# Optimization experiments

Measured on AMD Instinct MI355X. Metric: run time of the kernel, lower is better.

The kernel has to match this reference:

```python
import jax, jax.numpy as jnp
import numpy as np

D, H, DH, DF = 128, 8, 16, 512
N_Q, N_KV, E = 20000, 20000, 640000


def _xavier(key, shape):
    fan_in, fan_out = shape[1], shape[0]
    lim = float(np.sqrt(6.0 / (fan_in + fan_out)))
    return jax.random.uniform(key, shape, jnp.float32, -lim, lim)


def layer_norm(x, g, b, eps=1e-5):
    mu = jnp.mean(x, axis=-1, keepdims=True)
    var = jnp.var(x, axis=-1, keepdims=True)
    return (x - mu) * jax.lax.rsqrt(var + eps) * g + b


def setup_inputs() -> dict:
    key = jax.random.key(0)
    ks = jax.random.split(key, 12)
    return {
        "q_feat": jax.random.normal(ks[0], (N_Q, D), jnp.float32),
        "kv_feat": jax.random.normal(ks[1], (N_KV, D), jnp.float32),
        "src": jax.random.randint(ks[2], (E,), 0, N_KV, jnp.int32),
        "dst": jax.random.randint(ks[3], (E,), 0, N_Q, jnp.int32),
        "Wq": _xavier(ks[4], (H * DH, D)),
        "Wk": _xavier(ks[5], (H * DH, D)),
        "Wv": _xavier(ks[6], (H * DH, D)),
        "Wo": _xavier(ks[7], (D, H * DH)),
        "W1": _xavier(ks[8], (DF, D)),
        "bf1": jnp.zeros((DF,), jnp.float32),
        "W2": _xavier(ks[9], (D, DF)),
        "bf2": jnp.zeros((D,), jnp.float32),
        "ln1_g": jnp.ones((D,), jnp.float32),
        "ln1_b": jnp.zeros((D,), jnp.float32),
        "ln2_g": jnp.ones((D,), jnp.float32),
        "ln2_b": jnp.zeros((D,), jnp.float32),
    }


def reference(q_feat, kv_feat, src, dst, Wq, Wk, Wv, Wo, W1, bf1, W2, bf2,
              ln1_g, ln1_b, ln2_g, ln2_b):
    n_q = q_feat.shape[0]
    # projections -> [N, H, DH]
    q = (q_feat @ Wq.T).reshape(-1, H, DH)
    k = (kv_feat @ Wk.T).reshape(-1, H, DH)
    v = (kv_feat @ Wv.T).reshape(-1, H, DH)
    # edge scores: u_mul_v then sum over d_head, scaled (score per edge per head)
    score = jnp.einsum('ehd,ehd->eh', k[src], q[dst]) / np.sqrt(DH)
    # edge_softmax grouped by destination node
    mx = jax.ops.segment_max(score, dst, num_segments=n_q)  # [Nq, H]
    ex = jnp.exp(score - mx[dst])
    denom = jax.ops.segment_sum(ex, dst, num_segments=n_q)
    att = ex / denom[dst]  # [E, H]
    # weighted scatter-sum of values to destination nodes
    msg = v[src] * att[:, :, None]  # [E, H, DH]
    out = jax.ops.segment_sum(msg, dst, num_segments=n_q)  # [Nq, H, DH]
    sa = out.reshape(n_q, H * DH) @ Wo.T
    feat = layer_norm(q_feat + sa, ln1_g, ln1_b)
    ff = jax.nn.relu(feat @ W1.T + bf1) @ W2.T + bf2
    return layer_norm(feat + ff, ln2_g, ln2_b)
```

## Files before the change

kernel.cpp:

```cpp
#include <hip/hip_runtime.h>
#include <hip/hip_fp16.h>
#include <math.h>
#include <type_traits>

#define D 128
#define NH 8
#define DHD 16
#define DF 512
#define NSH 8
#define SSL 32

typedef _Float16 half8 __attribute__((ext_vector_type(8)));
typedef _Float16 half4 __attribute__((ext_vector_type(4)));
typedef float f32x4 __attribute__((ext_vector_type(4)));


__global__ __launch_bounds__(256) void mega_kernel(
    const float* __restrict__ q_feat, const float* __restrict__ kv_feat,
    const float* __restrict__ Wq, const float* __restrict__ Wk,
    const float* __restrict__ Wv,
    __half* __restrict__ fq, __half* __restrict__ fkv, int NQ, int NKV,
    const int* __restrict__ dst, const int* __restrict__ src,
    int* __restrict__ cnt, unsigned short* __restrict__ srcg, int E,
    const float* __restrict__ Wo, const float* __restrict__ W1,
    const float* __restrict__ W2,
    __half* __restrict__ wo16, __half* __restrict__ w116, __half* __restrict__ w216) {
    __shared__ __align__(16) __half As[64 * 128];
    __shared__ __align__(16) __half Ws[64 * 128];

    int xt = blockIdx.x;
    int tid = threadIdx.x;

    if (xt >= 2) {
        if (xt == (int)gridDim.x - 1) {
            int g = blockIdx.y * 256 + tid;
            if (g < 36864) {
                const float* s;
                __half* d;
                int idx = g;
                if (idx < 4096) { s = Wo; d = wo16; }
                else if (idx < 20480) { idx -= 4096; s = W1; d = w116; }
                else { idx -= 20480; s = W2; d = w216; }
                float4 f = ((const float4*)s)[idx];
                ushort4 o;
                o.x = __half_as_ushort(__float2half(f.x));
                o.y = __half_as_ushort(__float2half(f.y));
                o.z = __half_as_ushort(__float2half(f.z));
                o.w = __half_as_ushort(__float2half(f.w));
                ((ushort4*)d)[idx] = o;
            }
            return;
        }
        int b = (xt - 2) * gridDim.y + blockIdx.y;
        int sh = (blockIdx.y * gridDim.x + blockIdx.x) & (NSH - 1);
        int i4 = b * 256 + tid;
        int base = i4 << 2;
        if (base < E) {
            if (base + 3 < E) {
                int4 d4 = ((const int4*)dst)[i4];
                int4 s4 = ((const int4*)src)[i4];
                int dd[4] = {d4.x, d4.y, d4.z, d4.w};
                int ss[4] = {s4.x, s4.y, s4.z, s4.w};
#pragma unroll
                for (int u = 0; u < 4; ++u) {
                    int p = atomicAdd(&cnt[sh * NQ + dd[u]], 1);
                    if (p < SSL)
                        srcg[((size_t)dd[u] << 8) + (sh << 5) + p] = (unsigned short)ss[u];
                }
            } else {
                for (int u = 0; u < 4 && base + u < E; ++u) {
                    int dn = dst[base + u];
                    int sn = src[base + u];
                    int p = atomicAdd(&cnt[sh * NQ + dn], 1);
                    if (p < SSL)
                        srcg[((size_t)dn << 8) + (sh << 5) + p] = (unsigned short)sn;
                }
            }
        }
        return;
    }

    const float* A = xt ? kv_feat : q_feat;
    __half* C = xt ? fkv : fq;
    int O = xt ? 256 : 128;
    int NCT = xt ? 4 : 2;
    int N = xt ? NKV : NQ;
    int row0 = blockIdx.y * 64;
    if (row0 >= N) return;

    int lane = tid & 63;
    int w = tid >> 6;
    int l16 = lane & 15, lq = lane >> 4;

#pragma unroll
    for (int i = 0; i < 4; ++i) {
        int f = tid + i * 256;
        int ln = f & 63;
        int mt = (f >> 6) & 3;
        int kc = f >> 8;
        int m = row0 + mt * 16 + (ln & 15);
        int k = kc * 32 + (ln >> 4) * 8;
        half8 v = {};
        if (m < N) {
            const float4* p = (const float4*)(A + (size_t)m * 128 + k);
            float4 f0 = p[0], f1 = p[1];
            v = (half8){(_Float16)f0.x, (_Float16)f0.y, (_Float16)f0.z, (_Float16)f0.w,
                        (_Float16)f1.x, (_Float16)f1.y, (_Float16)f1.z, (_Float16)f1.w};
        }
        ((half8*)As)[f] = v;
    }

    for (int ct = 0; ct < NCT; ++ct) {
        __syncthreads();
#pragma unroll
        for (int i = 0; i < 4; ++i) {
            int f = tid + i * 256;
            int ln = f & 63;
            int nt = (f >> 6) & 3;
            int kc = f >> 8;
            int n = ct * 64 + nt * 16 + (ln & 15);
            int k = kc * 32 + (ln >> 4) * 8;
            const float* Wsrc;
            int r;
            if (xt == 0) {
                Wsrc = Wq; r = n;
            } else {
                int h = n >> 5, qd = (n >> 3) & 3, isv = (n >> 2) & 1, d2 = n & 3;
                r = h * 16 + qd * 4 + d2;
                Wsrc = isv ? Wv : Wk;
            }
            const float4* p = (const float4*)(Wsrc + (size_t)r * 128 + k);
            float4 f0 = p[0], f1 = p[1];
            ((half8*)Ws)[f] = (half8){(_Float16)f0.x, (_Float16)f0.y, (_Float16)f0.z, (_Float16)f0.w,
                                      (_Float16)f1.x, (_Float16)f1.y, (_Float16)f1.z, (_Float16)f1.w};
        }
        __syncthreads();
        f32x4 acc[4];
#pragma unroll
        for (int j = 0; j < 4; ++j) acc[j] = (f32x4){0.f, 0.f, 0.f, 0.f};
#pragma unroll
        for (int kc = 0; kc < 4; ++kc) {
            half8 a = ((half8*)As)[(kc * 4 + w) * 64 + lane];
            half8 b[4];
#pragma unroll
            for (int j = 0; j < 4; ++j) b[j] = ((half8*)Ws)[(kc * 4 + j) * 64 + lane];
#pragma unroll
            for (int j = 0; j < 4; ++j)
                acc[j] = __builtin_amdgcn_mfma_f32_16x16x32_f16(a, b[j], acc[j], 0, 0, 0);
        }
#pragma unroll
        for (int j = 0; j < 4; ++j) {
            int c = ct * 64 + j * 16 + l16;
#pragma unroll
            for (int r = 0; r < 4; ++r) {
                int row = row0 + w * 16 + lq * 4 + r;
                if (row < N) C[(size_t)row * O + c] = __float2half(acc[j][r]);
            }
        }
    }
}


__global__ __launch_bounds__(256) void attn_kernel(
    const __half* __restrict__ q, const __half* __restrict__ kv,
    const unsigned short* __restrict__ srcg, const int* __restrict__ cnt,
    __half* __restrict__ out, int NQ) {
    __shared__ unsigned short list[4][NSH * SSL];
    int wv = threadIdx.x >> 6;
    int n = blockIdx.x * 4 + wv;
    if (n >= NQ) return;
    int lane = threadIdx.x & 63;
    int eh = lane >> 5;
    int sub = lane & 31;
    int doff = sub << 2;

    int t0 = 0;
#pragma unroll
    for (int r = 0; r < NSH; ++r) {
        int cr = cnt[r * NQ + n];
        cr = cr < SSL ? cr : SSL;
        if (lane < cr)
            list[wv][t0 + lane] = srcg[((size_t)n << 8) + (r << 5) + lane];
        t0 += cr;
    }
    int total = t0;

    half4 q4 = *(const half4*)(q + (size_t)n * D + doff);
    float q0 = (float)q4[0] * 0.25f, q1 = (float)q4[1] * 0.25f;
    float q2 = (float)q4[2] * 0.25f, q3 = (float)q4[3] * 0.25f;
    float lA = 0.f, lB = 0.f, lC = 0.f, lD = 0.f;
    f32x4 aA = {0.f, 0.f, 0.f, 0.f}, aB = {0.f, 0.f, 0.f, 0.f};
    f32x4 aC = {0.f, 0.f, 0.f, 0.f}, aD = {0.f, 0.f, 0.f, 0.f};
    int j = 0;
    for (; j + 8 <= total; j += 8) {
        int e0 = list[wv][j + eh];
        int e1 = list[wv][j + 2 + eh];
        int e2 = list[wv][j + 4 + eh];
        int e3 = list[wv][j + 6 + eh];
        half8 c0 = *(const half8*)(kv + (size_t)e0 * 256 + (sub << 3));
        half8 c1 = *(const half8*)(kv + (size_t)e1 * 256 + (sub << 3));
        half8 c2 = *(const half8*)(kv + (size_t)e2 * 256 + (sub << 3));
        half8 c3 = *(const half8*)(kv + (size_t)e3 * 256 + (sub << 3));
        float p0 = q0 * (float)c0[0] + q1 * (float)c0[1] + q2 * (float)c0[2] + q3 * (float)c0[3];
        float p1 = q0 * (float)c1[0] + q1 * (float)c1[1] + q2 * (float)c1[2] + q3 * (float)c1[3];
        float p2 = q0 * (float)c2[0] + q1 * (float)c2[1] + q2 * (float)c2[2] + q3 * (float)c2[3];
        float p3 = q0 * (float)c3[0] + q1 * (float)c3[1] + q2 * (float)c3[2] + q3 * (float)c3[3];
        p0 += __shfl_xor(p0, 1, 4); p0 += __shfl_xor(p0, 2, 4);
        p1 += __shfl_xor(p1, 1, 4); p1 += __shfl_xor(p1, 2, 4);
        p2 += __shfl_xor(p2, 1, 4); p2 += __shfl_xor(p2, 2, 4);
        p3 += __shfl_xor(p3, 1, 4); p3 += __shfl_xor(p3, 2, 4);
        float x0 = __expf(fminf(p0, 70.f));
        float x1 = __expf(fminf(p1, 70.f));
        float x2 = __expf(fminf(p2, 70.f));
        float x3 = __expf(fminf(p3, 70.f));
        lA += x0; lB += x1; lC += x2; lD += x3;
        aA[0] += x0 * (float)c0[4]; aA[1] += x0 * (float)c0[5];
        aA[2] += x0 * (float)c0[6]; aA[3] += x0 * (float)c0[7];
        aB[0] += x1 * (float)c1[4]; aB[1] += x1 * (float)c1[5];
        aB[2] += x1 * (float)c1[6]; aB[3] += x1 * (float)c1[7];
        aC[0] += x2 * (float)c2[4]; aC[1] += x2 * (float)c2[5];
        aC[2] += x2 * (float)c2[6]; aC[3] += x2 * (float)c2[7];
        aD[0] += x3 * (float)c3[4]; aD[1] += x3 * (float)c3[5];
        aD[2] += x3 * (float)c3[6]; aD[3] += x3 * (float)c3[7];
    }
    for (; j + 4 <= total; j += 4) {
        int e0 = list[wv][j + eh];
        int e1 = list[wv][j + 2 + eh];
        half8 c0 = *(const half8*)(kv + (size_t)e0 * 256 + (sub << 3));
        half8 c1 = *(const half8*)(kv + (size_t)e1 * 256 + (sub << 3));
        float p0 = q0 * (float)c0[0] + q1 * (float)c0[1] + q2 * (float)c0[2] + q3 * (float)c0[3];
        float p1 = q0 * (float)c1[0] + q1 * (float)c1[1] + q2 * (float)c1[2] + q3 * (float)c1[3];
        p0 += __shfl_xor(p0, 1, 4); p0 += __shfl_xor(p0, 2, 4);
        p1 += __shfl_xor(p1, 1, 4); p1 += __shfl_xor(p1, 2, 4);
        float x0 = __expf(fminf(p0, 70.f));
        float x1 = __expf(fminf(p1, 70.f));
        lA += x0; lB += x1;
        aA[0] += x0 * (float)c0[4]; aA[1] += x0 * (float)c0[5];
        aA[2] += x0 * (float)c0[6]; aA[3] += x0 * (float)c0[7];
        aB[0] += x1 * (float)c1[4]; aB[1] += x1 * (float)c1[5];
        aB[2] += x1 * (float)c1[6]; aB[3] += x1 * (float)c1[7];
    }
    for (; j < total; j += 2) {
        bool valid = (j + eh) < total;
        int e0 = list[wv][valid ? (j + eh) : 0];
        half8 c0 = *(const half8*)(kv + (size_t)e0 * 256 + (sub << 3));
        float p0 = q0 * (float)c0[0] + q1 * (float)c0[1] + q2 * (float)c0[2] + q3 * (float)c0[3];
        p0 += __shfl_xor(p0, 1, 4); p0 += __shfl_xor(p0, 2, 4);
        float x0 = valid ? __expf(fminf(p0, 70.f)) : 0.f;
        lA += x0;
        aA[0] += x0 * (float)c0[4]; aA[1] += x0 * (float)c0[5];
        aA[2] += x0 * (float)c0[6]; aA[3] += x0 * (float)c0[7];
    }
    float l = (lA + lB) + (lC + lD);
    f32x4 a;
#pragma unroll
    for (int i = 0; i < 4; ++i) a[i] = (aA[i] + aB[i]) + (aC[i] + aD[i]);
    l += __shfl_xor(l, 32);
#pragma unroll
    for (int i = 0; i < 4; ++i) a[i] += __shfl_xor(a[i], 32);
    if (eh == 0) {
        float rl = (l > 0.f) ? 1.f / l : 0.f;
        half4 o = {(_Float16)(a[0] * rl), (_Float16)(a[1] * rl),
                   (_Float16)(a[2] * rl), (_Float16)(a[3] * rl)};
        *(half4*)(out + (size_t)n * D + doff) = o;
    }
}


__device__ __forceinline__ int feat_idx64(int rr, int mt, int c) {
    return (((c >> 5) * 4 + mt) * 64 + ((c >> 3) & 3) * 16 + rr) * 8 + (c & 7);
}

__global__ __launch_bounds__(256) void tail_kernel(
    const __half* __restrict__ A , const __half* __restrict__ Wo16,
    const float* __restrict__ res1 ,
    const float* __restrict__ g1, const float* __restrict__ b1,
    const __half* __restrict__ W1h, const float* __restrict__ fb1,
    const __half* __restrict__ W2h, const float* __restrict__ fb2,
    const float* __restrict__ g2, const float* __restrict__ b2,
    float* __restrict__ out, int N) {
    __shared__ __align__(16) __half Feat[64 * 128];
    __shared__ __align__(16) __half S1[64 * 128];
    __shared__ __align__(16) __half S2[128 * 64];
    __shared__ __align__(16) __half Hs[64 * 64];
    int tid = threadIdx.x, lane = tid & 63, w = tid >> 6;
    int row0 = blockIdx.x * 64;
    int l16 = lane & 15, lq = lane >> 4;

#pragma unroll
    for (int i = 0; i < 4; ++i) {
        int f = tid + i * 256;
        int ln = f & 63, mt = (f >> 6) & 3, kc = f >> 8;
        int m = row0 + mt * 16 + (ln & 15);
        int k = kc * 32 + (ln >> 4) * 8;
        half8 av = {};
        if (m < N) av = *(const half8*)(A + (size_t)m * D + k);
        ((half8*)S1)[f] = av;
    }

    f32x4 acc[8];
#pragma unroll
    for (int j = 0; j < 8; ++j) acc[j] = (f32x4){0.f, 0.f, 0.f, 0.f};
#pragma unroll
    for (int kt = 0; kt < 2; ++kt) {
        __syncthreads();
#pragma unroll
        for (int i = 0; i < 4; ++i) {
            int f = tid + i * 256;
            int ln = f & 63, ot = (f >> 6) & 7, kc2 = f >> 9;
            int o = ot * 16 + (ln & 15);
            int k = kt * 64 + kc2 * 32 + (ln >> 4) * 8;
            ((half8*)S2)[f] = *(const half8*)(Wo16 + (size_t)o * D + k);
        }
        __syncthreads();
#pragma unroll
        for (int kc2 = 0; kc2 < 2; ++kc2) {
            half8 a = ((half8*)S1)[((kt * 2 + kc2) * 4 + w) * 64 + lane];
            half8 bf[8];
#pragma unroll
            for (int j = 0; j < 8; ++j) bf[j] = ((half8*)S2)[(kc2 * 8 + j) * 64 + lane];
#pragma unroll
            for (int j = 0; j < 8; ++j)
                acc[j] = __builtin_amdgcn_mfma_f32_16x16x32_f16(a, bf[j], acc[j], 0, 0, 0);
        }
    }
    __syncthreads();

#pragma unroll
    for (int r = 0; r < 4; ++r) {
        int rr = lq * 4 + r;
        int row = row0 + w * 16 + rr;
        bool valid = row < N;
        float vals[8];
        float s = 0.f, sq = 0.f;
#pragma unroll
        for (int j = 0; j < 8; ++j) {
            int c = j * 16 + l16;
            float v = acc[j][r];
            if (valid) v += res1[(size_t)row * D + c];
            vals[j] = v;
            s += v;
            sq += v * v;
        }
#pragma unroll
        for (int m = 1; m < 16; m <<= 1) {
            s += __shfl_xor(s, m, 16);
            sq += __shfl_xor(sq, m, 16);
        }
        float mu = s * (1.f / 128.f);
        float var = sq * (1.f / 128.f) - mu * mu;
        float inv = rsqrtf(var + 1e-5f);
#pragma unroll
        for (int j = 0; j < 8; ++j) {
            int c = j * 16 + l16;
            float o = (vals[j] - mu) * inv * g1[c] + b1[c];
            Feat[feat_idx64(rr, w, c)] = __float2half(o);
        }
    }
    __syncthreads();

    half8 a_all[4];
#pragma unroll
    for (int kc = 0; kc < 4; ++kc)
        a_all[kc] = ((half8*)Feat)[(kc * 4 + w) * 64 + lane];

    f32x4 oacc[8];
#pragma unroll
    for (int j = 0; j < 8; ++j) oacc[j] = (f32x4){0.f, 0.f, 0.f, 0.f};

    for (int hc = 0; hc < 8; ++hc) {
        __syncthreads();
#pragma unroll
        for (int i = 0; i < 4; ++i) {
            int f = tid + i * 256;
            int ln = f & 63, nt = (f >> 6) & 3, kc = f >> 8;
            int n = hc * 64 + nt * 16 + (ln & 15);
            int k = kc * 32 + (ln >> 4) * 8;
            ((half8*)S1)[f] = *(const half8*)(W1h + (size_t)n * D + k);
        }
#pragma unroll
        for (int i = 0; i < 4; ++i) {
            int f = tid + i * 256;
            int ln = f & 63, ot = (f >> 6) & 7, kc2 = f >> 9;
            int o = ot * 16 + (ln & 15);
            int k = hc * 64 + kc2 * 32 + (ln >> 4) * 8;
            ((half8*)S2)[f] = *(const half8*)(W2h + (size_t)o * DF + k);
        }
        __syncthreads();
        f32x4 hacc[4];
#pragma unroll
        for (int j = 0; j < 4; ++j) hacc[j] = (f32x4){0.f, 0.f, 0.f, 0.f};
#pragma unroll
        for (int kc = 0; kc < 4; ++kc) {
            half8 b[4];
#pragma unroll
            for (int j = 0; j < 4; ++j) b[j] = ((half8*)S1)[(kc * 4 + j) * 64 + lane];
#pragma unroll
            for (int j = 0; j < 4; ++j)
                hacc[j] = __builtin_amdgcn_mfma_f32_16x16x32_f16(a_all[kc], b[j], hacc[j], 0, 0, 0);
        }
#pragma unroll
        for (int j = 0; j < 4; ++j) {
            float bias1 = fb1[hc * 64 + j * 16 + l16];
#pragma unroll
            for (int r = 0; r < 4; ++r) {
                float v = fmaxf(hacc[j][r] + bias1, 0.f);
                int kc2 = j >> 1;
                int lanep = ((j & 1) * 2 + (l16 >> 3)) * 16 + lq * 4 + r;
                Hs[((kc2 * 4 + w) * 64 + lanep) * 8 + (l16 & 7)] = __float2half(v);
            }
        }
        __syncthreads();
#pragma unroll
        for (int kc2 = 0; kc2 < 2; ++kc2) {
            half8 a = ((half8*)Hs)[(kc2 * 4 + w) * 64 + lane];
            half8 b[8];
#pragma unroll
            for (int ot = 0; ot < 8; ++ot) b[ot] = ((half8*)S2)[(kc2 * 8 + ot) * 64 + lane];
#pragma unroll
            for (int ot = 0; ot < 8; ++ot)
                oacc[ot] = __builtin_amdgcn_mfma_f32_16x16x32_f16(a, b[ot], oacc[ot], 0, 0, 0);
        }
    }

#pragma unroll
    for (int r = 0; r < 4; ++r) {
        int rr = lq * 4 + r;
        int row = row0 + w * 16 + rr;
        bool valid = row < N;
        float vals[8];
        float s = 0.f, sq = 0.f;
#pragma unroll
        for (int j = 0; j < 8; ++j) {
            int c = j * 16 + l16;
            float v = oacc[j][r] + fb2[c] + __half2float(Feat[feat_idx64(rr, w, c)]);
            vals[j] = v;
            s += v;
            sq += v * v;
        }
#pragma unroll
        for (int m = 1; m < 16; m <<= 1) {
            s += __shfl_xor(s, m, 16);
            sq += __shfl_xor(sq, m, 16);
        }
        float mu = s * (1.f / 128.f);
        float var = sq * (1.f / 128.f) - mu * mu;
        float inv = rsqrtf(var + 1e-5f);
        if (valid) {
#pragma unroll
            for (int j = 0; j < 8; ++j) {
                int c = j * 16 + l16;
                out[(size_t)row * D + c] = (vals[j] - mu) * inv * g2[c] + b2[c];
            }
        }
    }
}


extern "C" void kernel_launch(void* const* d_in, const int* in_sizes, int n_in,
                              void* d_out, int out_size, void* d_ws, size_t ws_size,
                              hipStream_t stream) {
    const float* q_feat = (const float*)d_in[0];
    const float* kv_feat = (const float*)d_in[1];
    const int* src = (const int*)d_in[2];
    const int* dst = (const int*)d_in[3];
    const float* Wq = (const float*)d_in[4];
    const float* Wk = (const float*)d_in[5];
    const float* Wv = (const float*)d_in[6];
    const float* Wo = (const float*)d_in[7];
    const float* W1 = (const float*)d_in[8];
    const float* bf1 = (const float*)d_in[9];
    const float* W2 = (const float*)d_in[10];
    const float* bf2 = (const float*)d_in[11];
    const float* ln1g = (const float*)d_in[12];
    const float* ln1b = (const float*)d_in[13];
    const float* ln2g = (const float*)d_in[14];
    const float* ln2b = (const float*)d_in[15];

    int NQ = in_sizes[0] / D;
    int NKV = in_sizes[1] / D;
    int E = in_sizes[2];
    float* out = (float*)d_out;

    char* base = (char*)d_ws;
    size_t off = 0;
    auto alloc = [&](size_t bytes) -> void* {
        void* p = base + off;
        off += (bytes + 255) & ~(size_t)255;
        return p;
    };
    __half* fq16 = (__half*)alloc((size_t)NQ * D * 2);
    __half* fkv = (__half*)alloc((size_t)NKV * 256 * 2);
    __half* fattn16 = (__half*)alloc((size_t)NQ * D * 2);
    int* cnt = (int*)alloc((size_t)NSH * NQ * 4);
    unsigned short* srcg = (unsigned short*)alloc((size_t)NQ * NSH * SSL * 2);
    __half* wo16 = (__half*)alloc((size_t)D * D * 2);
    __half* w116 = (__half*)alloc((size_t)DF * D * 2);
    __half* w216 = (__half*)alloc((size_t)D * DF * 2);

    hipMemsetAsync(cnt, 0, (size_t)NSH * NQ * sizeof(int), stream);

    dim3 blk(256);
    int NMX = NQ > NKV ? NQ : NKV;
    int ytiles = (NMX + 63) / 64;
    int fillBlocks = (E + 1023) / 1024;
    int fillPlanes = (fillBlocks + ytiles - 1) / ytiles;
    mega_kernel<<<dim3(3 + fillPlanes, ytiles), blk, 0, stream>>>(
        q_feat, kv_feat, Wq, Wk, Wv, fq16, fkv, NQ, NKV,
        dst, src, cnt, srcg, E, Wo, W1, W2, wo16, w116, w216);

    attn_kernel<<<(NQ + 3) / 4, blk, 0, stream>>>(fq16, fkv, srcg, cnt, fattn16, NQ);

    tail_kernel<<<(NQ + 63) / 64, blk, 0, stream>>>(
        fattn16, wo16, q_feat, ln1g, ln1b, w116, bf1, w216, bf2, ln2g, ln2b, out, NQ);
}
```

Measured before the change: 218.2 us.

## Split mega kernel into separate conv, fill and projection kernels; transpose count layout

Splits the fused mega kernel into three launches: weight fp16 conversion, edge bucketing fill, and Q/KV projection. The count array becomes node-major, so the attention kernel reads all eight shard counts with two int4 loads instead of eight strided loads. The per-shard slot capacity rises from 32 to 64, which doubles the srcg buffer but lowers the risk of dropping edges. The cost is extra launch overhead, and fill and projection can no longer overlap inside one grid.

```diff
diff --git a/kernel.cpp b/kernel.cpp
--- a/kernel.cpp
+++ b/kernel.cpp
@@ -8,77 +8,72 @@
 #define DHD 16
 #define DF 512
 #define NSH 8
-#define SSL 32
+#define SSL 64
 
 typedef _Float16 half8 __attribute__((ext_vector_type(8)));
 typedef _Float16 half4 __attribute__((ext_vector_type(4)));
 typedef float f32x4 __attribute__((ext_vector_type(4)));
 
-
-__global__ __launch_bounds__(256) void mega_kernel(
+__global__ __launch_bounds__(256) void conv_kernel(
+    const float* __restrict__ Wo, const float* __restrict__ W1,
+    const float* __restrict__ W2,
+    __half* __restrict__ wo16, __half* __restrict__ w116, __half* __restrict__ w216) {
+    int g = blockIdx.x * 256 + threadIdx.x;
+    if (g >= 36864) return;
+    const float* s;
+    __half* d;
+    int idx = g;
+    if (idx < 4096) { s = Wo; d = wo16; }
+    else if (idx < 20480) { idx -= 4096; s = W1; d = w116; }
+    else { idx -= 20480; s = W2; d = w216; }
+    float4 f = ((const float4*)s)[idx];
+    ushort4 o;
+    o.x = __half_as_ushort(__float2half(f.x));
+    o.y = __half_as_ushort(__float2half(f.y));
+    o.z = __half_as_ushort(__float2half(f.z));
+    o.w = __half_as_ushort(__float2half(f.w));
+    ((ushort4*)d)[idx] = o;
+}
+
+__global__ __launch_bounds__(256) void fill_kernel(
+    const int* __restrict__ dst, const int* __restrict__ src,
+    int* __restrict__ cnt, unsigned short* __restrict__ srcg, int E) {
+    int i4 = blockIdx.x * 256 + threadIdx.x;
+    int sh = blockIdx.x & (NSH - 1);
+    int base = i4 << 2;
+    if (base >= E) return;
+    if (base + 3 < E) {
+        int4 d4 = ((const int4*)dst)[i4];
+        int4 s4 = ((const int4*)src)[i4];
+        int dd[4] = {d4.x, d4.y, d4.z, d4.w};
+        int ss[4] = {s4.x, s4.y, s4.z, s4.w};
+#pragma unroll
+        for (int u = 0; u < 4; ++u) {
+            int p = atomicAdd(&cnt[dd[u] * NSH + sh], 1);
+            if (p < SSL)
+                srcg[((size_t)dd[u] << 9) + (sh << 6) + p] = (unsigned short)ss[u];
+        }
+    } else {
+        for (int u = 0; u < 4 && base + u < E; ++u) {
+            int dn = dst[base + u];
+            int sn = src[base + u];
+            int p = atomicAdd(&cnt[dn * NSH + sh], 1);
+            if (p < SSL)
+                srcg[((size_t)dn << 9) + (sh << 6) + p] = (unsigned short)sn;
+        }
+    }
+}
+
+__global__ __launch_bounds__(256) void proj_kernel(
     const float* __restrict__ q_feat, const float* __restrict__ kv_feat,
     const float* __restrict__ Wq, const float* __restrict__ Wk,
     const float* __restrict__ Wv,
-    __half* __restrict__ fq, __half* __restrict__ fkv, int NQ, int NKV,
-    const int* __restrict__ dst, const int* __restrict__ src,
-    int* __restrict__ cnt, unsigned short* __restrict__ srcg, int E,
-    const float* __restrict__ Wo, const float* __restrict__ W1,
-    const float* __restrict__ W2,
-    __half* __restrict__ wo16, __half* __restrict__ w116, __half* __restrict__ w216) {
+    __half* __restrict__ fq, __half* __restrict__ fkv, int NQ, int NKV) {
     __shared__ __align__(16) __half As[64 * 128];
     __shared__ __align__(16) __half Ws[64 * 128];
 
     int xt = blockIdx.x;
     int tid = threadIdx.x;
-
-    if (xt >= 2) {
-        if (xt == (int)gridDim.x - 1) {
-            int g = blockIdx.y * 256 + tid;
-            if (g < 36864) {
-                const float* s;
-                __half* d;
-                int idx = g;
-                if (idx < 4096) { s = Wo; d = wo16; }
-                else if (idx < 20480) { idx -= 4096; s = W1; d = w116; }
-                else { idx -= 20480; s = W2; d = w216; }
-                float4 f = ((const float4*)s)[idx];
-                ushort4 o;
-                o.x = __half_as_ushort(__float2half(f.x));
-                o.y = __half_as_ushort(__float2half(f.y));
-                o.z = __half_as_ushort(__float2half(f.z));
-                o.w = __half_as_ushort(__float2half(f.w));
-                ((ushort4*)d)[idx] = o;
-            }
-            return;
-        }
-        int b = (xt - 2) * gridDim.y + blockIdx.y;
-        int sh = (blockIdx.y * gridDim.x + blockIdx.x) & (NSH - 1);
-        int i4 = b * 256 + tid;
-        int base = i4 << 2;
-        if (base < E) {
-            if (base + 3 < E) {
-                int4 d4 = ((const int4*)dst)[i4];
-                int4 s4 = ((const int4*)src)[i4];
-                int dd[4] = {d4.x, d4.y, d4.z, d4.w};
-                int ss[4] = {s4.x, s4.y, s4.z, s4.w};
-#pragma unroll
-                for (int u = 0; u < 4; ++u) {
-                    int p = atomicAdd(&cnt[sh * NQ + dd[u]], 1);
-                    if (p < SSL)
-                        srcg[((size_t)dd[u] << 8) + (sh << 5) + p] = (unsigned short)ss[u];
-                }
-            } else {
-                for (int u = 0; u < 4 && base + u < E; ++u) {
-                    int dn = dst[base + u];
-                    int sn = src[base + u];
-                    int p = atomicAdd(&cnt[sh * NQ + dn], 1);
-                    if (p < SSL)
-                        srcg[((size_t)dn << 8) + (sh << 5) + p] = (unsigned short)sn;
-                }
-            }
-        }
-        return;
-    }
 
     const float* A = xt ? kv_feat : q_feat;
     __half* C = xt ? fkv : fq;
@@ -174,13 +169,15 @@
     int sub = lane & 31;
     int doff = sub << 2;
 
+    const int4* c4 = (const int4*)(cnt + n * NSH);
+    int4 ca = c4[0], cb = c4[1];
+    int cs[8] = {ca.x, ca.y, ca.z, ca.w, cb.x, cb.y, cb.z, cb.w};
     int t0 = 0;
 #pragma unroll
     for (int r = 0; r < NSH; ++r) {
-        int cr = cnt[r * NQ + n];
-        cr = cr < SSL ? cr : SSL;
+        int cr = cs[r] < SSL ? cs[r] : SSL;
         if (lane < cr)
-            list[wv][t0 + lane] = srcg[((size_t)n << 8) + (r << 5) + lane];
+            list[wv][t0 + lane] = srcg[((size_t)n << 9) + (r << 6) + lane];
         t0 += cr;
     }
     int total = t0;
@@ -492,22 +489,24 @@
     __half* fq16 = (__half*)alloc((size_t)NQ * D * 2);
     __half* fkv = (__half*)alloc((size_t)NKV * 256 * 2);
     __half* fattn16 = (__half*)alloc((size_t)NQ * D * 2);
-    int* cnt = (int*)alloc((size_t)NSH * NQ * 4);
+    int* cnt = (int*)alloc((size_t)NQ * NSH * 4);
     unsigned short* srcg = (unsigned short*)alloc((size_t)NQ * NSH * SSL * 2);
     __half* wo16 = (__half*)alloc((size_t)D * D * 2);
     __half* w116 = (__half*)alloc((size_t)DF * D * 2);
     __half* w216 = (__half*)alloc((size_t)D * DF * 2);
 
-    hipMemsetAsync(cnt, 0, (size_t)NSH * NQ * sizeof(int), stream);
+    hipMemsetAsync(cnt, 0, (size_t)NQ * NSH * sizeof(int), stream);
 
     dim3 blk(256);
+    conv_kernel<<<(36864 + 255) / 256, blk, 0, stream>>>(Wo, W1, W2, wo16, w116, w216);
+
+    int fillBlocks = (E + 1023) / 1024;
+    fill_kernel<<<fillBlocks, blk, 0, stream>>>(dst, src, cnt, srcg, E);
+
     int NMX = NQ > NKV ? NQ : NKV;
     int ytiles = (NMX + 63) / 64;
-    int fillBlocks = (E + 1023) / 1024;
-    int fillPlanes = (fillBlocks + ytiles - 1) / ytiles;
-    mega_kernel<<<dim3(3 + fillPlanes, ytiles), blk, 0, stream>>>(
-        q_feat, kv_feat, Wq, Wk, Wv, fq16, fkv, NQ, NKV,
-        dst, src, cnt, srcg, E, Wo, W1, W2, wo16, w116, w216);
+    proj_kernel<<<dim3(2, ytiles), blk, 0, stream>>>(
+        q_feat, kv_feat, Wq, Wk, Wv, fq16, fkv, NQ, NKV);
 
     attn_kernel<<<(NQ + 3) / 4, blk, 0, stream>>>(fq16, fkv, srcg, cnt, fattn16, NQ);
 
```

Result: slower. 228.0 us (+4.5%).
